# Kernel optimization log

Measured on AMD Instinct MI355X. Metric: run time of the kernel, lower is better.

The kernel has to match this reference:

```python
import jax, jax.numpy as jnp
import numpy as np

SEARCH_RANGE = 4  # matches argv.search_range


def setup_inputs() -> dict:
    key = jax.random.key(0)
    k1, k2 = jax.random.split(key)
    B, C, H, W = 8, 128, 128, 128
    first = jax.random.normal(k1, (B, C, H, W), dtype=jnp.float32)
    second = jax.random.normal(k2, (B, C, H, W), dtype=jnp.float32)
    return {"first": first, "second": second}


def reference(first, second):
    r = SEARCH_RANGE
    B, C, H, W = first.shape
    # pad last two dims (H, W) by search_range on each side, zeros
    padded = jnp.pad(second, ((0, 0), (0, 0), (r, r), (r, r)))
    max_offset = 2 * r + 1
    # For each static (y, x) offset, slice the shifted window and reduce over
    # channels: cost[b, y*max_offset + x, h, w] = mean_c first * padded_shifted.
    costs = [
        jnp.mean(first * jax.lax.dynamic_slice(padded, (0, 0, y, x), (B, C, H, W)), axis=1)
        for y in range(max_offset)
        for x in range(max_offset)
    ]
    return jnp.stack(costs, axis=1)  # [B, (2r+1)^2, H, W]
```

## Files before the change

### kernel.cpp

```cpp
#include <hip/hip_runtime.h>


constexpr int B = 8, C = 128, H = 128, W = 128;
constexpr int RNG = 4, MO = 9;
constexpr int RW  = 4;
constexpr int TH  = 2;
constexpr int HWc = H * W;
constexpr int SROWS = TH + 2 * RNG;
constexpr int SLAB  = SROWS * W;
constexpr int NBUF  = 4;

typedef float f32x4 __attribute__((ext_vector_type(4)));

__global__ __launch_bounds__(576)
__attribute__((amdgpu_waves_per_eu(2, 5)))
void corr_kernel(const float* __restrict__ first,
                 const float* __restrict__ second,
                 float* __restrict__ out)
{
    const int tx = threadIdx.x;
    const int hy = threadIdx.y;
    const int dz = threadIdx.z;
    const int h0 = blockIdx.x * TH;
    const int b  = blockIdx.y;
    const int w0 = tx * RW;
    const int lane = tx + 32 * hy;

    __shared__ __align__(16) float slab[NBUF][SLAB];

    const bool do_stage = (dz < 5);
    const float* gsrc = nullptr;
    int ldsoff = 0;
    if (do_stage) {
        const int r0 = h0 - RNG + 2 * dz;
        const int cs = r0 < 0 ? 0 : (r0 > H - 2 ? H - 2 : r0);
        gsrc  = second + (size_t)b * C * HWc + cs * W + lane * 4;
        ldsoff = 2 * dz * W;
    }

    const int  srow   = h0 + hy + dz - RNG;
    const bool rvalid = (srow >= 0) && (srow < H);
    const bool ledge  = (tx == 0);
    const bool redge  = (tx == 31);
    const int off0  = ledge ? 0       : (w0 - 4);
    const int off2  = redge ? (W - 8) : (w0 + 4);
    const int sbase = (hy + dz) * W;

    float acc[MO][RW];
#pragma unroll
    for (int i = 0; i < MO; ++i)
#pragma unroll
        for (int p = 0; p < RW; ++p) acc[i][p] = 0.0f;

#define STAGE(k)                                                            \
    if (do_stage) {                                                         \
        __builtin_amdgcn_global_load_lds(                                   \
            (const __attribute__((address_space(1))) void*)                 \
                (gsrc + (size_t)(k) * HWc),                                 \
            (__attribute__((address_space(3))) void*)                       \
                (&slab[(k) & (NBUF - 1)][ldsoff]),                          \
            16, 0, 0);                                                      \
    }

    const float* fp = first + (size_t)b * C * HWc + (h0 + hy) * W + w0;

    f32x4 fcur = *(const f32x4*)(fp);
    fp += HWc;

    STAGE(0)
    STAGE(1)

    for (int k = 0; k < C; ++k) {
        __syncthreads();

        if (k < C - 2) STAGE(k + 2)

        f32x4 fnxt;
        if (k < C - 1) { fnxt = *(const f32x4*)(fp); fp += HWc; }

        const float* sb = slab[k & (NBUF - 1)];
        f32x4 a0 = *(const f32x4*)(sb + sbase + off0);
        f32x4 a1 = *(const f32x4*)(sb + sbase + w0);
        f32x4 a2 = *(const f32x4*)(sb + sbase + off2);
        if (ledge) a0 = (f32x4){0.f, 0.f, 0.f, 0.f};
        if (redge) a2 = (f32x4){0.f, 0.f, 0.f, 0.f};
        const float s[12] = {a0.x, a0.y, a0.z, a0.w,
                             a1.x, a1.y, a1.z, a1.w,
                             a2.x, a2.y, a2.z, a2.w};
        const float fvv[RW] = {fcur.x, fcur.y, fcur.z, fcur.w};
#pragma unroll
        for (int dx = 0; dx < MO; ++dx)
#pragma unroll
            for (int p = 0; p < RW; ++p)
                acc[dx][p] += fvv[p] * s[p + dx];

        fcur = fnxt;
    }
#undef STAGE

    const float inv = rvalid ? (1.0f / (float)C) : 0.0f;
    float* obase = out + ((size_t)b * (MO * MO) + (size_t)dz * MO) * HWc
                       + (size_t)(h0 + hy) * W + w0;
#pragma unroll
    for (int dx = 0; dx < MO; ++dx) {
        f32x4 v = {acc[dx][0] * inv, acc[dx][1] * inv,
                   acc[dx][2] * inv, acc[dx][3] * inv};
        *(f32x4*)(obase + (size_t)dx * HWc) = v;
    }
}

extern "C" void kernel_launch(void* const* d_in, const int* in_sizes, int n_in,
                              void* d_out, int out_size, void* d_ws, size_t ws_size,
                              hipStream_t stream) {
    const float* first  = (const float*)d_in[0];
    const float* second = (const float*)d_in[1];
    float* out = (float*)d_out;

    dim3 grid(H / TH, B);
    dim3 block(32, TH, MO);
    corr_kernel<<<grid, block, 0, stream>>>(first, second, out);
}
```

Baseline: 223.4 us.

## Give each wave private LDS buffers and replace block barriers with vmcnt waits

Each of the nine waves in a block now stages its own two rows of `first` and two shifted rows of `second` into a private 4-deep LDS ring, using `global_load_lds`. Because each wave only reads data it staged itself, the per-channel `__syncthreads` is replaced by `s_waitcnt vmcnt` waits, with a three-deep prefetch and a peeled tail. The cost being targeted is block-wide barrier stalls across the 128-channel loop. In exchange, LDS use per block rises sharply, which can lower occupancy. Rows of `second` shared between waves are now loaded redundantly instead of once per block.

```diff
diff --git a/kernel.cpp b/kernel.cpp
--- a/kernel.cpp
+++ b/kernel.cpp
@@ -6,8 +6,8 @@
 constexpr int RW  = 4;
 constexpr int TH  = 2;
 constexpr int HWc = H * W;
-constexpr int SROWS = TH + 2 * RNG;
-constexpr int SLAB  = SROWS * W;
+constexpr int BROWS = 4;
+constexpr int BUFW  = BROWS * W;
 constexpr int NBUF  = 4;
 
 typedef float f32x4 __attribute__((ext_vector_type(4)));
@@ -26,25 +26,25 @@
     const int w0 = tx * RW;
     const int lane = tx + 32 * hy;
 
-    __shared__ __align__(16) float slab[NBUF][SLAB];
+    __shared__ __align__(16) float slab[MO][NBUF][BUFW];
 
-    const bool do_stage = (dz < 5);
-    const float* gsrc = nullptr;
-    int ldsoff = 0;
-    if (do_stage) {
-        const int r0 = h0 - RNG + 2 * dz;
-        const int cs = r0 < 0 ? 0 : (r0 > H - 2 ? H - 2 : r0);
-        gsrc  = second + (size_t)b * C * HWc + cs * W + lane * 4;
-        ldsoff = 2 * dz * W;
-    }
+    const int ls = lane >> 5;
+    const int lc = (lane & 31) * 4;
+    const float* gf = first + (size_t)b * C * HWc + (size_t)(h0 + ls) * W + lc;
+    const int  sr  = h0 + dz - RNG + ls;
+    const int  src = sr < 0 ? 0 : (sr > H - 1 ? H - 1 : sr);
+    const float* gs = second + (size_t)b * C * HWc + (size_t)src * W + lc;
+
+    float* mybuf = &slab[dz][0][0];
 
     const int  srow   = h0 + hy + dz - RNG;
     const bool rvalid = (srow >= 0) && (srow < H);
     const bool ledge  = (tx == 0);
     const bool redge  = (tx == 31);
-    const int off0  = ledge ? 0       : (w0 - 4);
-    const int off2  = redge ? (W - 8) : (w0 + 4);
-    const int sbase = (hy + dz) * W;
+    const int o_f  = hy * W + w0;
+    const int o_a1 = (2 + hy) * W + w0;
+    const int o_a0 = ledge ? o_a1 : (o_a1 - 4);
+    const int o_a2 = redge ? o_a1 : (o_a1 + 4);
 
     float acc[MO][RW];
 #pragma unroll
@@ -53,49 +53,59 @@
         for (int p = 0; p < RW; ++p) acc[i][p] = 0.0f;
 
 #define STAGE(k)                                                            \
-    if (do_stage) {                                                         \
+    {                                                                       \
+        float* db = mybuf + ((k) & (NBUF - 1)) * BUFW;                      \
         __builtin_amdgcn_global_load_lds(                                   \
             (const __attribute__((address_space(1))) void*)                 \
-                (gsrc + (size_t)(k) * HWc),                                 \
-            (__attribute__((address_space(3))) void*)                       \
-                (&slab[(k) & (NBUF - 1)][ldsoff]),                          \
+                (gf + (size_t)(k) * HWc),                                   \
+            (__attribute__((address_space(3))) void*)db, 16, 0, 0);         \
+        __builtin_amdgcn_global_load_lds(                                   \
+            (const __attribute__((address_space(1))) void*)                 \
+                (gs + (size_t)(k) * HWc),                                   \
+            (__attribute__((address_space(3))) void*)(db + 2 * W),          \
             16, 0, 0);                                                      \
     }
 
-    const float* fp = first + (size_t)b * C * HWc + (h0 + hy) * W + w0;
+#define COMPUTE(k)                                                         \
+    {                                                                       \
+        const float* sb = mybuf + ((k) & (NBUF - 1)) * BUFW;                \
+        f32x4 fv = *(const f32x4*)(sb + o_f);                               \
+        f32x4 a0 = *(const f32x4*)(sb + o_a0);                              \
+        f32x4 a1 = *(const f32x4*)(sb + o_a1);                              \
+        f32x4 a2 = *(const f32x4*)(sb + o_a2);                              \
+        if (ledge) a0 = (f32x4){0.f, 0.f, 0.f, 0.f};                        \
+        if (redge) a2 = (f32x4){0.f, 0.f, 0.f, 0.f};                        \
+        const float s[12]  = {a0.x, a0.y, a0.z, a0.w,                       \
+                              a1.x, a1.y, a1.z, a1.w,                       \
+                              a2.x, a2.y, a2.z, a2.w};                      \
+        const float fvv[RW] = {fv.x, fv.y, fv.z, fv.w};                     \
+        _Pragma("unroll")                                                   \
+        for (int dx = 0; dx < MO; ++dx)                                     \
+            _Pragma("unroll")                                               \
+            for (int p = 0; p < RW; ++p)                                    \
+                acc[dx][p] += fvv[p] * s[p + dx];                           \
+    }
 
-    f32x4 fcur = *(const f32x4*)(fp);
-    fp += HWc;
+#define VWAIT(N)                                                            \
+    asm volatile("s_waitcnt vmcnt(" #N ")" ::: "memory");                   \
+    __builtin_amdgcn_sched_barrier(0);
 
     STAGE(0)
     STAGE(1)
+    STAGE(2)
 
-    for (int k = 0; k < C; ++k) {
-        __syncthreads();
+#pragma unroll 4
+    for (int k = 0; k < C - 3; ++k) {
+        VWAIT(4)
+        STAGE(k + 3)
+        COMPUTE(k)
+    }
+    VWAIT(4)  COMPUTE(C - 3)
+    VWAIT(2)  COMPUTE(C - 2)
+    VWAIT(0)  COMPUTE(C - 1)
 
-        if (k < C - 2) STAGE(k + 2)
-
-        f32x4 fnxt;
-        if (k < C - 1) { fnxt = *(const f32x4*)(fp); fp += HWc; }
-
-        const float* sb = slab[k & (NBUF - 1)];
-        f32x4 a0 = *(const f32x4*)(sb + sbase + off0);
-        f32x4 a1 = *(const f32x4*)(sb + sbase + w0);
-        f32x4 a2 = *(const f32x4*)(sb + sbase + off2);
-        if (ledge) a0 = (f32x4){0.f, 0.f, 0.f, 0.f};
-        if (redge) a2 = (f32x4){0.f, 0.f, 0.f, 0.f};
-        const float s[12] = {a0.x, a0.y, a0.z, a0.w,
-                             a1.x, a1.y, a1.z, a1.w,
-                             a2.x, a2.y, a2.z, a2.w};
-        const float fvv[RW] = {fcur.x, fcur.y, fcur.z, fcur.w};
-#pragma unroll
-        for (int dx = 0; dx < MO; ++dx)
-#pragma unroll
-            for (int p = 0; p < RW; ++p)
-                acc[dx][p] += fvv[p] * s[p + dx];
-
-        fcur = fnxt;
-    }
+#undef VWAIT
+#undef COMPUTE
 #undef STAGE
 
     const float inv = rvalid ? (1.0f / (float)C) : 0.0f;
```

Result: faster. 194.6 us (-12.9%).
